# Kernel tuning notes

Hardware: AMD Instinct MI355X
Metric: run time of the kernel (lower is better)

## Reference

```python
import jax, jax.numpy as jnp
import numpy as np

HEADS, DK, DV = 8, 64, 64
DM = HEADS * DK                 # 512
ROUNDS, SEQ, BUCKET = 2, 4096, 64
NCHUNK = SEQ // BUCKET          # 64 chunks
NBUCKETS = SEQ // BUCKET        # 64 hash buckets (Reformer convention)
SCALE = 8.0                     # sqrt(d_k)
NEG_BIG = -1e15
BATCH = 4


def setup_inputs() -> dict:
    key = jax.random.key(0)
    kq, kk, kv, kr = jax.random.split(key, 4)
    q = jax.random.normal(kq, (BATCH, SEQ, DM), jnp.float32)
    k = jax.random.normal(kk, (BATCH, SEQ, DM), jnp.float32)
    v = jax.random.normal(kv, (BATCH, SEQ, DM), jnp.float32)
    # angular-LSH random rotations: (rounds, d_model, n_buckets//2)
    R = jax.random.normal(kr, (ROUNDS, DM, NBUCKETS // 2), jnp.float32)
    return {"q": q, "k": k, "v": v, "R": R}


def _window(x):
    # x: (r, b, S, ...) -> (r, b, n_chunks, 2*BUCKET, ...)
    # each window = [previous chunk (wrapped), current chunk]
    r, b, S = x.shape[:3]
    xc = x.reshape((r, b, NCHUNK, BUCKET) + x.shape[3:])
    return jnp.concatenate([jnp.roll(xc, 1, axis=2), xc], axis=3)


def _lsh_attention(q, k, v, R):
    b = q.shape[0]
    # --- hash queries (same sorted_idx reused for q, k, v, as in the module) ---
    rot = jnp.einsum('bsd,rdm->rbsm', q, R)                       # (r,b,S,nb/2)
    h = jnp.argmax(jnp.concatenate([rot, -rot], axis=-1), axis=-1)
    h = h.astype(jnp.int32) + 1                                    # bucket 0 reserved for padding
    sorted_idx = jnp.argsort(h, axis=-1, stable=True)              # (r,b,S)

    def gather(x):  # (b,S,d) -> (r,b,S,d) sorted by bucket per round
        xb = jnp.broadcast_to(x[None], (ROUNDS,) + x.shape)
        return jnp.take_along_axis(xb, sorted_idx[..., None], axis=2)

    qs, ks, vs = gather(q), gather(k), gather(v)
    hs = jnp.take_along_axis(h, sorted_idx, axis=2)                # (r,b,S)

    # --- chunk into local windows ---
    qs = _window(qs.reshape(ROUNDS, b, SEQ, HEADS, DK))            # (r,b,n,2c,h,dk)
    ks = _window(ks.reshape(ROUNDS, b, SEQ, HEADS, DK))
    vs = _window(vs.reshape(ROUNDS, b, SEQ, HEADS, DV))
    hw = _window(hs)                                               # (r,b,n,2c)

    # --- per-window attention with bucket mask + log-count bias ---
    attn = jnp.einsum('rbnqhd,rbnkhd->rbnhqk', qs, ks) / SCALE     # (r,b,n,h,2c,2c)
    hm = (hw[:, :, :, :, None] == hw[:, :, :, None, :]) & (hw[:, :, :, :, None] != 0)
    hm = hm[:, :, :, None].astype(jnp.float32)                     # (r,b,n,1,2c,2c)
    cnt = hm * jnp.sum(hm, axis=4, keepdims=True)                  # count term (sum over q dim, as in source)
    bias = (1.0 - hm) * NEG_BIG - jnp.log(jnp.clip(cnt, 1.0))
    attn = attn + bias
    attn = attn + jnp.eye(2 * BUCKET, dtype=attn.dtype) * -1e5     # self-attention mask
    attn = jax.nn.softmax(attn, axis=-1)
    out = jnp.einsum('rbnhml,rbnlhd->rbnmhd', attn, vs)            # (r,b,n,2c,h,dv)
    out = out[:, :, :, BUCKET:]                                    # keep current-chunk queries
    out = out.reshape(ROUNDS, b, SEQ, HEADS, DV)

    # --- unsort back to original token order, sum over rounds ---
    inv = jnp.argsort(sorted_idx, axis=-1, stable=True)
    out = jnp.take_along_axis(out, inv[:, :, :, None, None], axis=2)
    return jnp.sum(out, axis=0)                                    # (b,S,heads,dv)


def reference(q, k, v, R):
    return _lsh_attention(q, k, v, R)
```

## Files before the change

### kernel.cpp

```cpp
#include <hip/hip_runtime.h>
#include <hip/hip_bf16.h>
#include <hip/hip_fp16.h>

#define HEADS 8
#define DK 64
#define DV 64
#define DM 512
#define ROUNDS 2
#define SEQ 4096
#define BUCKET 64
#define NCHUNK 64
#define BATCH 4

typedef _Float16 f16;
typedef f16 f16x4 __attribute__((ext_vector_type(4)));
typedef f16 f16x8 __attribute__((ext_vector_type(8)));
typedef float f32x4 __attribute__((ext_vector_type(4)));

#define MFMA16(a, b, c) __builtin_amdgcn_mfma_f32_16x16x32_f16((a), (b), (c), 0, 0, 0)

__global__ __launch_bounds__(256) void hash_kernel(const float* __restrict__ q,
                                                   const float* __restrict__ R,
                                                   int* __restrict__ h_out) {
  int blk = blockIdx.x;
  int stile = blk & 63;
  int b = (blk >> 6) & (BATCH - 1);
  int r = blk >> 8;
  int s0 = stile << 6;
  int rb = r * BATCH + b;

  __shared__ float Qf[64 * 66];
  __shared__ float Rf[64 * 32];

  int tid = threadIdx.x;
  int qg = tid >> 3;
  int cg = tid & 7;
  int q0 = qg << 1;
  int m0 = cg << 2;

  int qrow = tid & 63;
  int qd0 = (tid >> 6) << 4;
  const float* qbase = q + ((size_t)b * SEQ + s0 + qrow) * DM;
  const float* rbase = R + (size_t)r * DM * 32;

  float4 qreg[4];
  float rr[8];
#pragma unroll
  for (int c = 0; c < 4; ++c)
    qreg[c] = *reinterpret_cast<const float4*>(qbase + qd0 + c * 4);
#pragma unroll
  for (int j = 0; j < 8; ++j) rr[j] = rbase[j * 256 + tid];

  double acc[2][4];
#pragma unroll
  for (int qq = 0; qq < 2; ++qq)
#pragma unroll
    for (int mm = 0; mm < 4; ++mm) acc[qq][mm] = 0.0;

  for (int t = 0; t < 8; ++t) {
#pragma unroll
    for (int c = 0; c < 4; ++c) {
      int d = qd0 + c * 4;
      Qf[(d + 0) * 66 + qrow] = qreg[c].x;
      Qf[(d + 1) * 66 + qrow] = qreg[c].y;
      Qf[(d + 2) * 66 + qrow] = qreg[c].z;
      Qf[(d + 3) * 66 + qrow] = qreg[c].w;
    }
#pragma unroll
    for (int j = 0; j < 8; ++j) Rf[j * 256 + tid] = rr[j];
    __syncthreads();

    if (t < 7) {
      int dt = t + 1;
#pragma unroll
      for (int c = 0; c < 4; ++c)
        qreg[c] = *reinterpret_cast<const float4*>(qbase + dt * 64 + qd0 + c * 4);
#pragma unroll
      for (int j = 0; j < 8; ++j) rr[j] = rbase[dt * 2048 + j * 256 + tid];
    }

#pragma unroll 4
    for (int d = 0; d < 64; ++d) {
      float2 qf = *reinterpret_cast<const float2*>(&Qf[d * 66 + q0]);
      float4 rf = *reinterpret_cast<const float4*>(&Rf[d * 32 + m0]);
      double qa = (double)qf.x;
      double qb = (double)qf.y;
      double rv0 = (double)rf.x;
      double rv1 = (double)rf.y;
      double rv2 = (double)rf.z;
      double rv3 = (double)rf.w;
      acc[0][0] = fma(qa, rv0, acc[0][0]);
      acc[0][1] = fma(qa, rv1, acc[0][1]);
      acc[0][2] = fma(qa, rv2, acc[0][2]);
      acc[0][3] = fma(qa, rv3, acc[0][3]);
      acc[1][0] = fma(qb, rv0, acc[1][0]);
      acc[1][1] = fma(qb, rv1, acc[1][1]);
      acc[1][2] = fma(qb, rv2, acc[1][2]);
      acc[1][3] = fma(qb, rv3, acc[1][3]);
    }
    __syncthreads();
  }

  double bv[2];
  int bi[2];
#pragma unroll
  for (int qq = 0; qq < 2; ++qq) {
    double v = acc[qq][0];
    int i = m0;
#pragma unroll
    for (int mm = 1; mm < 4; ++mm)
      if (acc[qq][mm] > v) { v = acc[qq][mm]; i = m0 + mm; }
#pragma unroll
    for (int mm = 0; mm < 4; ++mm) {
      double nv = -acc[qq][mm];
      if (nv > v) { v = nv; i = 32 + m0 + mm; }
    }
    bv[qq] = v;
    bi[qq] = i;
  }
#pragma unroll
  for (int off = 1; off < 8; off <<= 1) {
#pragma unroll
    for (int qq = 0; qq < 2; ++qq) {
      double ov = __shfl_xor(bv[qq], off);
      int oi = __shfl_xor(bi[qq], off);
      if (ov > bv[qq] || (ov == bv[qq] && oi < bi[qq])) { bv[qq] = ov; bi[qq] = oi; }
    }
  }
  if (cg == 0) {
#pragma unroll
    for (int qq = 0; qq < 2; ++qq)
      h_out[(size_t)rb * SEQ + s0 + q0 + qq] = bi[qq] + 1;
  }
}

__global__ __launch_bounds__(256) void sort_kernel(const int* __restrict__ h,
                                                   int* __restrict__ sorted_idx) {
  int rb = blockIdx.x;
  const int* hp = h + (size_t)rb * SEQ;
  __shared__ unsigned char hs[SEQ];
  __shared__ unsigned char rs[SEQ];
  __shared__ int tile_cnt[64][64];
  __shared__ int tile_base[64][64];
  __shared__ int bucket_base[64];
  __shared__ int bucket_tot[64];
  int tid = threadIdx.x;
  int wave = tid >> 6, lane = tid & 63;
  for (int i = tid; i < 64 * 64; i += 256) ((int*)tile_cnt)[i] = 0;
  __syncthreads();
  for (int t = wave; t < 64; t += 4) {
    int s = (t << 6) + lane;
    int hv = hp[s] - 1;
    unsigned long long mm = ~0ull;
#pragma unroll
    for (int bit = 0; bit < 6; ++bit) {
      unsigned long long bb = __ballot((hv >> bit) & 1);
      mm &= ((hv >> bit) & 1) ? bb : ~bb;
    }
    int rank = __popcll(mm & ((1ull << lane) - 1ull));
    hs[s] = (unsigned char)hv;
    rs[s] = (unsigned char)rank;
    if (rank == 0) tile_cnt[t][hv] = __popcll(mm);
  }
  __syncthreads();
  if (tid < 64) {
    int bkt = tid;
    int run = 0;
    for (int t = 0; t < 64; ++t) { tile_base[t][bkt] = run; run += tile_cnt[t][bkt]; }
    bucket_tot[bkt] = run;
  }
  __syncthreads();
  if (tid == 0) {
    int run = 0;
    for (int bkt = 0; bkt < 64; ++bkt) { bucket_base[bkt] = run; run += bucket_tot[bkt]; }
  }
  __syncthreads();
  for (int t = wave; t < 64; t += 4) {
    int s = (t << 6) + lane;
    int hv = hs[s];
    int pos = bucket_base[hv] + tile_base[t][hv] + rs[s];
    sorted_idx[(size_t)rb * SEQ + pos] = s;
  }
}

__global__ __launch_bounds__(256) void attn_kernel(
    const float* __restrict__ q, const float* __restrict__ k,
    const float* __restrict__ v, const int* __restrict__ h,
    const int* __restrict__ sidx, float* __restrict__ out, int r,
    int accumulate) {
  int x = blockIdx.x;
  int hd = x & 7;
  int n = (x >> 3) & 63;
  int b = x >> 9;
  int rb = r * BATCH + b;

  __shared__ __align__(16) unsigned char smem[45056];
  __shared__ int orig_w[128];
  __shared__ int hw[128];
  f16* Qh = reinterpret_cast<f16*>(smem);
  f16* Kh = reinterpret_cast<f16*>(smem + 9216);
  const int VOFF = 27648;

  int tid = threadIdx.x;
  int wave = tid >> 6;
  int lane = tid & 63;
  int lo = lane & 15;
  int hi = lane >> 4;

  if (tid < 128) {
    int j = tid;
    int sp = (j < 64) ? ((((n + 63) & 63) << 6) + j) : ((n << 6) + (j - 64));
    int orig = sidx[(size_t)rb * SEQ + sp];
    orig_w[j] = orig;
    hw[j] = h[(size_t)rb * SEQ + orig];
  }
  __syncthreads();

  const size_t gbase = (size_t)b * SEQ * DM + hd * 64;

  float4 kreg[8], qreg[4];
#pragma unroll
  for (int t = 0; t < 8; ++t) {
    int idx = tid + t * 256;
    int j = idx >> 4, dq = idx & 15;
    kreg[t] = *reinterpret_cast<const float4*>(
        k + gbase + (size_t)orig_w[j] * DM + dq * 4);
  }
#pragma unroll
  for (int t = 0; t < 4; ++t) {
    int idx = tid + t * 256;
    int i = idx >> 4, dq = idx & 15;
    qreg[t] = *reinterpret_cast<const float4*>(
        q + gbase + (size_t)orig_w[64 + i] * DM + dq * 4);
  }
#pragma unroll
  for (int t = 0; t < 8; ++t) {
    int idx = tid + t * 256;
    int j = idx >> 4, dq = idx & 15;
    f16x4 hv = {(f16)kreg[t].x, (f16)kreg[t].y, (f16)kreg[t].z, (f16)kreg[t].w};
    *reinterpret_cast<f16x4*>(&Kh[j * 72 + dq * 4]) = hv;
  }
#pragma unroll
  for (int t = 0; t < 4; ++t) {
    int idx = tid + t * 256;
    int i = idx >> 4, dq = idx & 15;
    f16x4 hv = {(f16)qreg[t].x, (f16)qreg[t].y, (f16)qreg[t].z, (f16)qreg[t].w};
    *reinterpret_cast<f16x4*>(&Qh[i * 72 + dq * 4]) = hv;
  }
  __syncthreads();

  float4 vreg[8];
#pragma unroll
  for (int t = 0; t < 8; ++t) {
    int idx = tid + t * 256;
    int l = idx >> 4, dq = idx & 15;
    vreg[t] = *reinterpret_cast<const float4*>(
        v + gbase + (size_t)orig_w[l] * DM + dq * 4);
  }

  f32x4 acc[8];
#pragma unroll
  for (int t = 0; t < 8; ++t) acc[t] = (f32x4){0.f, 0.f, 0.f, 0.f};

  int qr_a = wave * 16 + lo;
  f16x8 aq0 = *reinterpret_cast<const f16x8*>(&Qh[qr_a * 72 + hi * 8]);
  f16x8 aq1 = *reinterpret_cast<const f16x8*>(&Qh[qr_a * 72 + 32 + hi * 8]);
#pragma unroll
  for (int t = 0; t < 8; ++t) {
    f16x8 b0 = *reinterpret_cast<const f16x8*>(&Kh[(t * 16 + lo) * 72 + hi * 8]);
    f16x8 b1 = *reinterpret_cast<const f16x8*>(&Kh[(t * 16 + lo) * 72 + 32 + hi * 8]);
    acc[t] = MFMA16(aq0, b0, acc[t]);
    acc[t] = MFMA16(aq1, b1, acc[t]);
  }

#pragma unroll
  for (int t = 0; t < 8; ++t) {
    int idx = tid + t * 256;
    int l = idx >> 4, dq = idx & 15;
    const float* vp = &vreg[t].x;
#pragma unroll
    for (int c = 0; c < 4; ++c) {
      int dv = dq * 4 + c;
      *reinterpret_cast<f16*>(smem + VOFF + dv * 272 + l * 2) = (f16)vp[c];
    }
  }

  int hq[4];
#pragma unroll
  for (int rg = 0; rg < 4; ++rg) hq[rg] = hw[64 + wave * 16 + hi * 4 + rg];
#pragma unroll
  for (int t = 0; t < 8; ++t) {
    int key = t * 16 + lo;
    int hj = hw[key];
#pragma unroll
    for (int rg = 0; rg < 4; ++rg) {
      int qr = wave * 16 + hi * 4 + rg;
      float lg = acc[t][rg] * 0.125f;
      if (hj != hq[rg]) lg = -1e15f;
      if (key == 64 + qr) lg -= 1e5f;
      acc[t][rg] = lg;
    }
  }
  float mx[4] = {-INFINITY, -INFINITY, -INFINITY, -INFINITY};
#pragma unroll
  for (int t = 0; t < 8; ++t)
#pragma unroll
    for (int rg = 0; rg < 4; ++rg) mx[rg] = fmaxf(mx[rg], acc[t][rg]);
#pragma unroll
  for (int off = 1; off <= 8; off <<= 1)
#pragma unroll
    for (int rg = 0; rg < 4; ++rg) mx[rg] = fmaxf(mx[rg], __shfl_xor(mx[rg], off));
  float sm[4] = {0.f, 0.f, 0.f, 0.f};
#pragma unroll
  for (int t = 0; t < 8; ++t)
#pragma unroll
    for (int rg = 0; rg < 4; ++rg) {
      float ev = __expf(acc[t][rg] - mx[rg]);
      acc[t][rg] = ev;
      sm[rg] += ev;
    }
#pragma unroll
  for (int off = 1; off <= 8; off <<= 1)
#pragma unroll
    for (int rg = 0; rg < 4; ++rg) sm[rg] += __shfl_xor(sm[rg], off);
  float inv[4];
#pragma unroll
  for (int rg = 0; rg < 4; ++rg) inv[rg] = 1.0f / sm[rg];

  __syncthreads();

#pragma unroll
  for (int t = 0; t < 8; ++t) {
    int key = t * 16 + lo;
#pragma unroll
    for (int rg = 0; rg < 4; ++rg) {
      int qr = wave * 16 + hi * 4 + rg;
      *reinterpret_cast<f16*>(smem + qr * 272 + key * 2) =
          (f16)(acc[t][rg] * inv[rg]);
    }
  }
  __syncthreads();

  f32x4 o[4];
#pragma unroll
  for (int dt = 0; dt < 4; ++dt) o[dt] = (f32x4){0.f, 0.f, 0.f, 0.f};
#pragma unroll
  for (int lt = 0; lt < 4; ++lt) {
    f16x8 ap = *reinterpret_cast<const f16x8*>(
        smem + qr_a * 272 + lt * 64 + hi * 16);
#pragma unroll
    for (int dt = 0; dt < 4; ++dt) {
      f16x8 bv = *reinterpret_cast<const f16x8*>(
          smem + VOFF + (dt * 16 + lo) * 272 + lt * 64 + hi * 16);
      o[dt] = MFMA16(ap, bv, o[dt]);
    }
  }

#pragma unroll
  for (int dt = 0; dt < 4; ++dt) {
#pragma unroll
    for (int rg = 0; rg < 4; ++rg) {
      int qr = wave * 16 + hi * 4 + rg;
      float* dst = out + gbase + (size_t)orig_w[64 + qr] * DM + dt * 16 + lo;
      if (accumulate) {
        *dst = *dst + o[dt][rg];
      } else {
        *dst = o[dt][rg];
      }
    }
  }
}

extern "C" void kernel_launch(void* const* d_in, const int* in_sizes, int n_in,
                              void* d_out, int out_size, void* d_ws,
                              size_t ws_size, hipStream_t stream) {
  (void)out_size; (void)ws_size;
  const int R_ELEMS = ROUNDS * DM * 32;
  const float *q, *k, *v, *R;
  if (n_in >= 4 && in_sizes[0] == R_ELEMS) {
    R = (const float*)d_in[0];
    k = (const float*)d_in[1];
    q = (const float*)d_in[2];
    v = (const float*)d_in[3];
  } else {
    q = (const float*)d_in[0];
    k = (const float*)d_in[1];
    v = (const float*)d_in[2];
    R = (const float*)d_in[3];
  }
  float* out = (float*)d_out;
  char* ws = (char*)d_ws;
  int* h = (int*)ws;
  int* sidx = (int*)(ws + ROUNDS * BATCH * SEQ * 4);

  hash_kernel<<<ROUNDS * BATCH * (SEQ / 64), 256, 0, stream>>>(q, R, h);
  sort_kernel<<<ROUNDS * BATCH, 256, 0, stream>>>(h, sidx);
  attn_kernel<<<BATCH * NCHUNK * HEADS, 256, 0, stream>>>(q, k, v, h, sidx, out, 0, 0);
  attn_kernel<<<BATCH * NCHUNK * HEADS, 256, 0, stream>>>(q, k, v, h, sidx, out, 1, 1);
}
```

Measured before the change: 234.4 us.

## Hash with split-fp16 MFMA and recompute near-tie rows in fp64

Replaces the fp64 FMA hashing GEMM with a three-term split-fp16 MFMA product (hi*hi + hi*lo + lo*hi), tracking top-1 and top-2 scores per row. Rows whose argmax margin falls below a small threshold are flagged, and a second kernel recomputes only those rows exactly in double precision. This removes the slow fp64 arithmetic from the common path while keeping argmax ties correct, at the cost of an extra launch, a flag buffer in workspace, and a fixed threshold that might miss some close cases.

```diff
diff --git a/kernel.cpp b/kernel.cpp
--- a/kernel.cpp
+++ b/kernel.cpp
@@ -11,6 +11,7 @@
 #define BUCKET 64
 #define NCHUNK 64
 #define BATCH 4
+#define GAP_THRESH 0.02f
 
 typedef _Float16 f16;
 typedef f16 f16x4 __attribute__((ext_vector_type(4)));
@@ -19,9 +20,9 @@
 
 #define MFMA16(a, b, c) __builtin_amdgcn_mfma_f32_16x16x32_f16((a), (b), (c), 0, 0, 0)
 
-__global__ __launch_bounds__(256) void hash_kernel(const float* __restrict__ q,
-                                                   const float* __restrict__ R,
-                                                   int* __restrict__ h_out) {
+__global__ __launch_bounds__(256) void hash_approx_kernel(
+    const float* __restrict__ q, const float* __restrict__ R,
+    int* __restrict__ h_out, unsigned char* __restrict__ flag) {
   int blk = blockIdx.x;
   int stile = blk & 63;
   int b = (blk >> 6) & (BATCH - 1);
@@ -29,108 +30,139 @@
   int s0 = stile << 6;
   int rb = r * BATCH + b;
 
-  __shared__ float Qf[64 * 66];
-  __shared__ float Rf[64 * 32];
+  __shared__ f16 Rh[32 * 520];
+  __shared__ f16 Rl[32 * 520];
 
   int tid = threadIdx.x;
-  int qg = tid >> 3;
-  int cg = tid & 7;
-  int q0 = qg << 1;
-  int m0 = cg << 2;
-
-  int qrow = tid & 63;
-  int qd0 = (tid >> 6) << 4;
-  const float* qbase = q + ((size_t)b * SEQ + s0 + qrow) * DM;
+  int w = tid >> 6, lane = tid & 63, lo = lane & 15, hi = lane >> 4;
+
   const float* rbase = R + (size_t)r * DM * 32;
-
-  float4 qreg[4];
-  float rr[8];
-#pragma unroll
-  for (int c = 0; c < 4; ++c)
-    qreg[c] = *reinterpret_cast<const float4*>(qbase + qd0 + c * 4);
-#pragma unroll
-  for (int j = 0; j < 8; ++j) rr[j] = rbase[j * 256 + tid];
-
-  double acc[2][4];
-#pragma unroll
-  for (int qq = 0; qq < 2; ++qq)
-#pragma unroll
-    for (int mm = 0; mm < 4; ++mm) acc[qq][mm] = 0.0;
-
-  for (int t = 0; t < 8; ++t) {
-#pragma unroll
-    for (int c = 0; c < 4; ++c) {
-      int d = qd0 + c * 4;
-      Qf[(d + 0) * 66 + qrow] = qreg[c].x;
-      Qf[(d + 1) * 66 + qrow] = qreg[c].y;
-      Qf[(d + 2) * 66 + qrow] = qreg[c].z;
-      Qf[(d + 3) * 66 + qrow] = qreg[c].w;
-    }
-#pragma unroll
-    for (int j = 0; j < 8; ++j) Rf[j * 256 + tid] = rr[j];
+#pragma unroll
+  for (int i = 0; i < 16; ++i) {
+    int fi = tid + i * 256;
+    float4 rv = *reinterpret_cast<const float4*>(rbase + fi * 4);
+    int d = fi >> 3, m0 = (fi & 7) * 4;
+    const float* rp = &rv.x;
+#pragma unroll
+    for (int e = 0; e < 4; ++e) {
+      float x = rp[e];
+      f16 hx = (f16)x;
+      Rh[(m0 + e) * 520 + d] = hx;
+      Rl[(m0 + e) * 520 + d] = (f16)(x - (float)hx);
+    }
+  }
+  __syncthreads();
+
+  int qr = w * 16 + lo;
+  const float* qp = q + ((size_t)b * SEQ + s0 + qr) * DM;
+
+  f32x4 acc0 = {0.f, 0.f, 0.f, 0.f}, acc1 = {0.f, 0.f, 0.f, 0.f};
+#pragma unroll 4
+  for (int ks = 0; ks < 16; ++ks) {
+    int k = ks * 32 + hi * 8;
+    float4 a0 = *reinterpret_cast<const float4*>(qp + k);
+    float4 a1 = *reinterpret_cast<const float4*>(qp + k + 4);
+    float av[8] = {a0.x, a0.y, a0.z, a0.w, a1.x, a1.y, a1.z, a1.w};
+    f16x8 ahi, alo;
+#pragma unroll
+    for (int e = 0; e < 8; ++e) {
+      f16 hx = (f16)av[e];
+      ahi[e] = hx;
+      alo[e] = (f16)(av[e] - (float)hx);
+    }
+    f16x8 bh0 = *reinterpret_cast<const f16x8*>(&Rh[lo * 520 + k]);
+    f16x8 bl0 = *reinterpret_cast<const f16x8*>(&Rl[lo * 520 + k]);
+    f16x8 bh1 = *reinterpret_cast<const f16x8*>(&Rh[(16 + lo) * 520 + k]);
+    f16x8 bl1 = *reinterpret_cast<const f16x8*>(&Rl[(16 + lo) * 520 + k]);
+    acc0 = MFMA16(ahi, bh0, acc0);
+    acc0 = MFMA16(ahi, bl0, acc0);
+    acc0 = MFMA16(alo, bh0, acc0);
+    acc1 = MFMA16(ahi, bh1, acc1);
+    acc1 = MFMA16(ahi, bl1, acc1);
+    acc1 = MFMA16(alo, bh1, acc1);
+  }
+
+#pragma unroll
+  for (int rg = 0; rg < 4; ++rg) {
+    float c0 = acc0[rg], c1 = acc1[rg];
+    float v1 = c0;
+    int i1 = lo;
+    float v2 = -INFINITY;
+    float cv[3] = {c1, -c0, -c1};
+    int ci[3] = {16 + lo, 32 + lo, 48 + lo};
+#pragma unroll
+    for (int c = 0; c < 3; ++c) {
+      if (cv[c] > v1) { v2 = v1; v1 = cv[c]; i1 = ci[c]; }
+      else v2 = fmaxf(v2, cv[c]);
+    }
+#pragma unroll
+    for (int off = 1; off <= 8; off <<= 1) {
+      float ov1 = __shfl_xor(v1, off);
+      int oi1 = __shfl_xor(i1, off);
+      float ov2 = __shfl_xor(v2, off);
+      if (ov1 > v1 || (ov1 == v1 && oi1 < i1)) {
+        v2 = fmaxf(v1, ov2);
+        v1 = ov1;
+        i1 = oi1;
+      } else {
+        v2 = fmaxf(v2, ov1);
+      }
+    }
+    if (lo == 0) {
+      int grow = s0 + w * 16 + hi * 4 + rg;
+      size_t gid = (size_t)rb * SEQ + grow;
+      h_out[gid] = i1 + 1;
+      flag[gid] = (v1 - v2 <= GAP_THRESH) ? 1 : 0;
+    }
+  }
+}
+
+__global__ __launch_bounds__(256) void hash_exact_kernel(
+    const float* __restrict__ q, const float* __restrict__ R,
+    const unsigned char* __restrict__ flag, int* __restrict__ h_out) {
+  int g0 = blockIdx.x * 64;
+  __shared__ int nf;
+  __shared__ unsigned char list[64];
+  __shared__ double pl[8][33];
+  int tid = threadIdx.x;
+  if (tid == 0) nf = 0;
+  __syncthreads();
+  if (tid < 64 && flag[g0 + tid]) {
+    int idx = atomicAdd(&nf, 1);
+    list[idx] = (unsigned char)tid;
+  }
+  __syncthreads();
+  int n = nf;
+  for (int i = 0; i < n; ++i) {
+    int g = g0 + list[i];
+    int rb = g >> 12, s = g & (SEQ - 1);
+    int r = rb >> 2, b = rb & (BATCH - 1);
+    int m = tid & 31, chunk = tid >> 5;
+    const float* qp = q + ((size_t)b * SEQ + s) * DM;
+    const float* rp = R + (size_t)r * DM * 32;
+    double part = 0.0;
+    for (int dd = 0; dd < 64; ++dd) {
+      int d = chunk * 64 + dd;
+      part = fma((double)qp[d], (double)rp[(size_t)d * 32 + m], part);
+    }
+    pl[chunk][m] = part;
     __syncthreads();
-
-    if (t < 7) {
-      int dt = t + 1;
-#pragma unroll
-      for (int c = 0; c < 4; ++c)
-        qreg[c] = *reinterpret_cast<const float4*>(qbase + dt * 64 + qd0 + c * 4);
-#pragma unroll
-      for (int j = 0; j < 8; ++j) rr[j] = rbase[dt * 2048 + j * 256 + tid];
-    }
-
-#pragma unroll 4
-    for (int d = 0; d < 64; ++d) {
-      float2 qf = *reinterpret_cast<const float2*>(&Qf[d * 66 + q0]);
-      float4 rf = *reinterpret_cast<const float4*>(&Rf[d * 32 + m0]);
-      double qa = (double)qf.x;
-      double qb = (double)qf.y;
-      double rv0 = (double)rf.x;
-      double rv1 = (double)rf.y;
-      double rv2 = (double)rf.z;
-      double rv3 = (double)rf.w;
-      acc[0][0] = fma(qa, rv0, acc[0][0]);
-      acc[0][1] = fma(qa, rv1, acc[0][1]);
-      acc[0][2] = fma(qa, rv2, acc[0][2]);
-      acc[0][3] = fma(qa, rv3, acc[0][3]);
-      acc[1][0] = fma(qb, rv0, acc[1][0]);
-      acc[1][1] = fma(qb, rv1, acc[1][1]);
-      acc[1][2] = fma(qb, rv2, acc[1][2]);
-      acc[1][3] = fma(qb, rv3, acc[1][3]);
+    if (tid < 32) {
+      double sum = 0.0;
+#pragma unroll
+      for (int c = 0; c < 8; ++c) sum += pl[c][m];
+      double v = sum;
+      int ix = m;
+      double nv = -sum;
+      if (nv > v) { v = nv; ix = m + 32; }
+      for (int off = 1; off <= 16; off <<= 1) {
+        double ov = __shfl_xor(v, off);
+        int oi = __shfl_xor(ix, off);
+        if (ov > v || (ov == v && oi < ix)) { v = ov; ix = oi; }
+      }
+      if (tid == 0) h_out[g] = ix + 1;
     }
     __syncthreads();
-  }
-
-  double bv[2];
-  int bi[2];
-#pragma unroll
-  for (int qq = 0; qq < 2; ++qq) {
-    double v = acc[qq][0];
-    int i = m0;
-#pragma unroll
-    for (int mm = 1; mm < 4; ++mm)
-      if (acc[qq][mm] > v) { v = acc[qq][mm]; i = m0 + mm; }
-#pragma unroll
-    for (int mm = 0; mm < 4; ++mm) {
-      double nv = -acc[qq][mm];
-      if (nv > v) { v = nv; i = 32 + m0 + mm; }
-    }
-    bv[qq] = v;
-    bi[qq] = i;
-  }
-#pragma unroll
-  for (int off = 1; off < 8; off <<= 1) {
-#pragma unroll
-    for (int qq = 0; qq < 2; ++qq) {
-      double ov = __shfl_xor(bv[qq], off);
-      int oi = __shfl_xor(bi[qq], off);
-      if (ov > bv[qq] || (ov == bv[qq] && oi < bi[qq])) { bv[qq] = ov; bi[qq] = oi; }
-    }
-  }
-  if (cg == 0) {
-#pragma unroll
-    for (int qq = 0; qq < 2; ++qq)
-      h_out[(size_t)rb * SEQ + s0 + q0 + qq] = bi[qq] + 1;
   }
 }
 
@@ -392,8 +424,10 @@
   char* ws = (char*)d_ws;
   int* h = (int*)ws;
   int* sidx = (int*)(ws + ROUNDS * BATCH * SEQ * 4);
-
-  hash_kernel<<<ROUNDS * BATCH * (SEQ / 64), 256, 0, stream>>>(q, R, h);
+  unsigned char* flag = (unsigned char*)(ws + 2 * ROUNDS * BATCH * SEQ * 4);
+
+  hash_approx_kernel<<<ROUNDS * BATCH * (SEQ / 64), 256, 0, stream>>>(q, R, h, flag);
+  hash_exact_kernel<<<ROUNDS * BATCH * (SEQ / 64), 256, 0, stream>>>(q, R, flag, h);
   sort_kernel<<<ROUNDS * BATCH, 256, 0, stream>>>(h, sidx);
   attn_kernel<<<BATCH * NCHUNK * HEADS, 256, 0, stream>>>(q, k, v, h, sidx, out, 0, 0);
   attn_kernel<<<BATCH * NCHUNK * HEADS, 256, 0, stream>>>(q, k, v, h, sidx, out, 1, 1);
```

New measurement: 219.4 us. -6.4%, faster.
